# Kernel optimization log

Hardware: AMD Instinct MI355X
Metric: run time of the kernel (lower is better)

The kernel has to match this reference:

```python
import jax, jax.numpy as jnp
import numpy as np

H, D = 16, 64            # total_num_heads, head_dim
E = H * D                # embed_dim = 1024
NUM_BUCKETS, MAX_DIST = 32, 128
SCALING = D ** -0.5


def _rel_buckets(seq_len):
    # WavLM bidirectional relative position buckets (static, computed in numpy)
    ctx = np.arange(seq_len)[:, None]
    mem = np.arange(seq_len)[None, :]
    rel = mem - ctx                                  # [s, s]
    nb = NUM_BUCKETS // 2
    buckets = (rel > 0).astype(np.int64) * nb
    rp = np.abs(rel)
    max_exact = nb // 2
    is_small = rp < max_exact
    large = max_exact + (
        np.log(np.maximum(rp, 1) / max_exact) / np.log(MAX_DIST / max_exact) * (nb - max_exact)
    ).astype(np.int64)
    large = np.minimum(large, nb - 1)
    buckets = buckets + np.where(is_small, rp, large)
    return jnp.asarray(buckets)


def setup_inputs() -> dict:
    key = jax.random.key(0)
    ks = jax.random.split(key, 12)
    s = 0.02
    x = jax.random.normal(ks[0], (8, 1024, E), jnp.float32)
    Wq = jax.random.normal(ks[1], (E, H * D), jnp.float32) * s
    bq = jnp.zeros((H * D,), jnp.float32)
    Wk = jax.random.normal(ks[2], (E, H * D), jnp.float32) * s
    bk = jnp.zeros((H * D,), jnp.float32)
    Wv = jax.random.normal(ks[3], (E, H * D), jnp.float32) * s
    bv = jnp.zeros((H * D,), jnp.float32)
    Wo = jax.random.normal(ks[4], (H * D, E), jnp.float32) * s
    bo = jnp.zeros((E,), jnp.float32)
    rel_embed = jax.random.normal(ks[5], (NUM_BUCKETS, H), jnp.float32) * s
    gru_w = jax.random.normal(ks[6], (D, 8), jnp.float32) * s
    gru_b = jnp.zeros((8,), jnp.float32)
    gru_const = jnp.ones((1, H, 1, 1), jnp.float32)
    return {"x": x, "Wq": Wq, "bq": bq, "Wk": Wk, "bk": bk, "Wv": Wv, "bv": bv,
            "Wo": Wo, "bo": bo, "rel_embed": rel_embed,
            "gru_w": gru_w, "gru_b": gru_b, "gru_const": gru_const}


def reference(x, Wq, bq, Wk, bk, Wv, bv, Wo, bo, rel_embed, gru_w, gru_b, gru_const):
    b, s, e = x.shape
    # relative position bias: [H, s, s]
    buckets = _rel_buckets(s)
    pos_bias = jnp.transpose(rel_embed[buckets], (2, 0, 1))
    # gated relative position (gru_rel_pos)
    qlayer = x.reshape(b, s, H, D).transpose(0, 2, 1, 3)            # [b,H,s,D]
    g = jnp.einsum('bhsd,de->bhse', qlayer, gru_w) + gru_b          # [b,H,s,8]
    g = jax.nn.sigmoid(g.reshape(b, H, s, 2, 4).sum(-1))           # [b,H,s,2]
    gate_a, gate_b = g[..., :1], g[..., 1:]                         # [b,H,s,1]
    gate = gate_a * (gate_b * gru_const - 1.0) + 2.0                # [b,H,s,1]
    bias = gate * pos_bias[None]                                    # [b,H,s,s]
    # projections -> [b,H,s,D]
    q = (x @ Wq + bq).reshape(b, s, H, D).transpose(0, 2, 1, 3)
    k = (x @ Wk + bk).reshape(b, s, H, D).transpose(0, 2, 1, 3)
    v = (x @ Wv + bv).reshape(b, s, H, D).transpose(0, 2, 1, 3)
    scores = SCALING * jnp.einsum('bhqd,bhkd->bhqk', q, k) + bias
    w = jax.nn.softmax(scores, axis=-1)   # includes stable max-subtract
    out = jnp.einsum('bhqk,bhkd->bhqd', w, v)
    out = out.transpose(0, 2, 1, 3).reshape(b, s, H * D)
    return out @ Wo + bo
```

## Files before the change

### kernel.cpp

```cpp
#include <hip/hip_runtime.h>
#include <hip/hip_bf16.h>
#include <math.h>


typedef __attribute__((ext_vector_type(8))) short short8;
typedef __attribute__((ext_vector_type(4))) float f32x4;

#define LDSP(p) ((__attribute__((address_space(3))) void*)(p))
#define GLBP(p) ((const __attribute__((address_space(1))) void*)(p))

__device__ __forceinline__ void async_ld16(const void* src, void* dst) {
  __builtin_amdgcn_global_load_lds(GLBP(src), LDSP(dst), 16, 0, 0);
}
__device__ __forceinline__ unsigned short f2bf(float f) {
  __hip_bfloat16 h = __float2bfloat16(f);
  return __builtin_bit_cast(unsigned short, h);
}

__global__ void prep_btab(const float* __restrict__ rel_embed,
                          float* __restrict__ btab) {
  const int idx = blockIdx.x * 256 + threadIdx.x;
  if (idx >= 2047) return;
  const int rel = idx - 1023;
  int bucket = (rel > 0) ? 16 : 0;
  const int rp = rel < 0 ? -rel : rel;
  if (rp < 8) {
    bucket += rp;
  } else {
    const double lv = log((double)rp / 8.0) / log(16.0) * 8.0;
    int large = 8 + (int)lv;
    bucket += (large < 15) ? large : 15;
  }
  #pragma unroll
  for (int h = 0; h < 16; ++h)
    btab[h * 2048 + idx] = rel_embed[bucket * 16 + h];
}

__global__ __launch_bounds__(256) void cvt_gate(
    const float* __restrict__ x, const float* __restrict__ gw,
    const float* __restrict__ gb, const float* __restrict__ gcst,
    unsigned short* __restrict__ xb, float* __restrict__ gate_ws) {
  __shared__ __align__(16) float xr[1024];
  const int bs = blockIdx.x, t = threadIdx.x;
  const float4 v = *(const float4*)&x[(size_t)bs * 1024 + t * 4];
  *(float4*)&xr[t * 4] = v;
  ushort4 o;
  o.x = f2bf(v.x); o.y = f2bf(v.y); o.z = f2bf(v.z); o.w = f2bf(v.w);
  *(ushort4*)&xb[(size_t)bs * 1024 + t * 4] = o;
  __syncthreads();
  const int h = t >> 4, i = t & 15;
  float pa = 0.f, pb = 0.f;
  #pragma unroll
  for (int j = 0; j < 4; ++j) {
    const int d = i * 4 + j;
    const float xv = xr[h * 64 + d];
    const float* wr = &gw[d * 8];
    pa += xv * (wr[0] + wr[1] + wr[2] + wr[3]);
    pb += xv * (wr[4] + wr[5] + wr[6] + wr[7]);
  }
  #pragma unroll
  for (int msk = 1; msk <= 8; msk <<= 1) {
    pa += __shfl_xor(pa, msk);
    pb += __shfl_xor(pb, msk);
  }
  if (i == 0) {
    const float ba = gb[0] + gb[1] + gb[2] + gb[3];
    const float bb = gb[4] + gb[5] + gb[6] + gb[7];
    const float ga  = 1.f / (1.f + __expf(-(pa + ba)));
    const float gbv = 1.f / (1.f + __expf(-(pb + bb)));
    const float gv  = ga * (gbv * gcst[h] - 1.f) + 2.f;
    const int b = bs >> 10, s = bs & 1023;
    gate_ws[(b * 16 + h) * 1024 + s] = gv;
  }
}

__global__ __launch_bounds__(256) void transW4(
    const float* __restrict__ W0, const float* __restrict__ W1,
    const float* __restrict__ W2, const float* __restrict__ W3,
    unsigned short* __restrict__ Wt_all) {
  __shared__ __align__(16) float tile[64][68];
  const int z = blockIdx.z;
  const float* W = (z == 0) ? W0 : (z == 1) ? W1 : (z == 2) ? W2 : W3;
  unsigned short* Wt = Wt_all + (size_t)z * 1048576;
  const int n0 = blockIdx.x * 64, k0 = blockIdx.y * 64;
  const int c = (threadIdx.x & 15) * 4, r = threadIdx.x >> 4;
  #pragma unroll
  for (int i = 0; i < 4; ++i)
    *(float4*)&tile[r + i * 16][c] =
        *(const float4*)&W[(size_t)(k0 + r + i * 16) * 1024 + n0 + c];
  __syncthreads();
  #pragma unroll
  for (int i = 0; i < 4; ++i) {
    const int n = r + i * 16;
    ushort4 o;
    o.x = f2bf(tile[c + 0][n]); o.y = f2bf(tile[c + 1][n]);
    o.z = f2bf(tile[c + 2][n]); o.w = f2bf(tile[c + 3][n]);
    *(ushort4*)&Wt[(size_t)(n0 + n) * 1024 + k0 + c] = o;
  }
}

__device__ __forceinline__ void gemm_core(
    const unsigned short* __restrict__ A, const unsigned short* __restrict__ Bt,
    unsigned short* As, unsigned short* Bs, const int m0, const int n0,
    f32x4 acc[4][4]) {
  const int t = threadIdx.x, w = t >> 6, l = t & 63;
  const int lr = l & 15, lg = l >> 4;
  const int wr = w >> 1, wc = w & 1;

  const unsigned short* asrc[4];
  const unsigned short* bsrc[4];
  unsigned short* adst[4];
  unsigned short* bdst[4];
  #pragma unroll
  for (int i = 0; i < 4; ++i) {
    const int p = (w * 4 + i) * 64 + l, r = p >> 3, c = p & 7;
    const int cs = c ^ (r & 7);
    asrc[i] = A + (size_t)(m0 + r) * 1024 + cs * 8;
    bsrc[i] = Bt + (size_t)(n0 + r) * 1024 + cs * 8;
    adst[i] = &As[(w * 4 + i) * 512];
    bdst[i] = &Bs[(w * 4 + i) * 512];
  }

  int offA[2][4], offB[2][4];
  #pragma unroll
  for (int ks = 0; ks < 2; ++ks)
    #pragma unroll
    for (int mt = 0; mt < 4; ++mt) {
      offA[ks][mt] = (wr * 64 + mt * 16 + lr) * 64 + ((ks * 4 + lg) ^ (lr & 7)) * 8;
      offB[ks][mt] = (wc * 64 + mt * 16 + lr) * 64 + ((ks * 4 + lg) ^ (lr & 7)) * 8;
    }

  for (int k0 = 0; k0 < 16; ++k0) {
    #pragma unroll
    for (int i = 0; i < 4; ++i) {
      async_ld16(asrc[i], adst[i]);
      async_ld16(bsrc[i], bdst[i]);
      asrc[i] += 64;
      bsrc[i] += 64;
    }
    __syncthreads();
    #pragma unroll
    for (int ks = 0; ks < 2; ++ks) {
      short8 af[4], bf[4];
      #pragma unroll
      for (int mt = 0; mt < 4; ++mt) af[mt] = *(const short8*)&As[offA[ks][mt]];
      #pragma unroll
      for (int nt = 0; nt < 4; ++nt) bf[nt] = *(const short8*)&Bs[offB[ks][nt]];
      #pragma unroll
      for (int mt = 0; mt < 4; ++mt)
        #pragma unroll
        for (int nt = 0; nt < 4; ++nt)
          acc[mt][nt] = __builtin_amdgcn_mfma_f32_16x16x32_bf16(
              af[mt], bf[nt], acc[mt][nt], 0, 0, 0);
    }
    __syncthreads();
  }
}

__global__ __launch_bounds__(256) void gemm_qkv(
    const unsigned short* __restrict__ A, const unsigned short* __restrict__ wt_all,
    const float* __restrict__ bq, const float* __restrict__ bk,
    const float* __restrict__ bv, unsigned short* __restrict__ q_ws,
    unsigned short* __restrict__ k_ws, unsigned short* __restrict__ vt_ws) {
  __shared__ __align__(16) unsigned short As[128 * 64];
  __shared__ __align__(16) unsigned short Bs[128 * 64];
  const int which = blockIdx.y >> 3;
  const int m0 = blockIdx.x * 128, n0 = (blockIdx.y & 7) * 128;
  const unsigned short* Bt = wt_all + (size_t)which * 1048576;
  const float* bias = (which == 0) ? bq : (which == 1) ? bk : bv;

  f32x4 acc[4][4];
  #pragma unroll
  for (int mt = 0; mt < 4; ++mt)
    #pragma unroll
    for (int nt = 0; nt < 4; ++nt) acc[mt][nt] = (f32x4){0.f, 0.f, 0.f, 0.f};
  gemm_core(A, Bt, As, Bs, m0, n0, acc);

  const int t = threadIdx.x, w = t >> 6, l = t & 63;
  const int lr = l & 15, lg = l >> 4;
  const int wr = w >> 1, wc = w & 1;
  const int mbase = m0 + wr * 64, nbase = n0 + wc * 64;

  if (which == 2) {
    #pragma unroll
    for (int mt = 0; mt < 4; ++mt) {
      const int m4 = mbase + mt * 16 + lg * 4;
      const int b = m4 >> 10, s = m4 & 1023;
      #pragma unroll
      for (int nt = 0; nt < 4; ++nt) {
        const int n = nbase + nt * 16 + lr, h = n >> 6, d = n & 63;
        const float bvv = bias[n];
        ushort4 o;
        o.x = f2bf(acc[mt][nt][0] + bvv);
        o.y = f2bf(acc[mt][nt][1] + bvv);
        o.z = f2bf(acc[mt][nt][2] + bvv);
        o.w = f2bf(acc[mt][nt][3] + bvv);
        *(ushort4*)&vt_ws[(size_t)(b * 16 + h) * 65536 + (size_t)d * 1024 + s] = o;
      }
    }
  } else {
    unsigned short* dst = (which == 0) ? q_ws : k_ws;
    const float scale = (which == 0) ? 0.125f : 1.0f;
    #pragma unroll
    for (int mt = 0; mt < 4; ++mt)
      #pragma unroll
      for (int nt = 0; nt < 4; ++nt) {
        const int n = nbase + nt * 16 + lr, h = n >> 6, d = n & 63;
        const float bvv = bias[n];
        #pragma unroll
        for (int i = 0; i < 4; ++i) {
          const int m = mbase + mt * 16 + lg * 4 + i;
          const int b = m >> 10, s = m & 1023;
          dst[(size_t)(b * 16 + h) * 65536 + s * 64 + d] =
              f2bf((acc[mt][nt][i] + bvv) * scale);
        }
      }
  }
}

__global__ __launch_bounds__(256) void gemm_out(
    const unsigned short* __restrict__ A, const unsigned short* __restrict__ Bt,
    const float* __restrict__ bias, float* __restrict__ C) {
  __shared__ __align__(16) unsigned short As[128 * 64];
  __shared__ __align__(16) unsigned short Bs[128 * 64];
  const int m0 = blockIdx.x * 128, n0 = blockIdx.y * 128;
  f32x4 acc[4][4];
  #pragma unroll
  for (int mt = 0; mt < 4; ++mt)
    #pragma unroll
    for (int nt = 0; nt < 4; ++nt) acc[mt][nt] = (f32x4){0.f, 0.f, 0.f, 0.f};
  gemm_core(A, Bt, As, Bs, m0, n0, acc);

  const int t = threadIdx.x, w = t >> 6, l = t & 63;
  const int lr = l & 15, lg = l >> 4;
  const int wr = w >> 1, wc = w & 1;
  const int mbase = m0 + wr * 64, nbase = n0 + wc * 64;
  #pragma unroll
  for (int mt = 0; mt < 4; ++mt)
    #pragma unroll
    for (int nt = 0; nt < 4; ++nt) {
      const int n = nbase + nt * 16 + lr;
      const float bvv = bias[n];
      #pragma unroll
      for (int i = 0; i < 4; ++i) {
        const int m = mbase + mt * 16 + lg * 4 + i;
        C[(size_t)m * 1024 + n] = acc[mt][nt][i] + bvv;
      }
    }
}

__global__ __launch_bounds__(256) void attn_mfma(
    const unsigned short* __restrict__ q_ws, const unsigned short* __restrict__ k_ws,
    const unsigned short* __restrict__ vt_ws, const float* __restrict__ gate_ws,
    const float* __restrict__ btab, unsigned short* __restrict__ ctx) {
  __shared__ __align__(16) unsigned short Ks[2][64 * 64];
  __shared__ __align__(16) unsigned short Vts[2][64 * 64];
  __shared__ __align__(16) unsigned short QPs[64 * 64];
  __shared__ __align__(16) float biasl[1088];
  __shared__ float gates[64];
  __shared__ float scl[64];

  const int t = threadIdx.x, w = t >> 6, l = t & 63;
  const int lr = l & 15, lg = l >> 4;
  const int bh = blockIdx.x, h = bh & 15, b = bh >> 4;
  const int q0 = blockIdx.y * 64;
  const size_t hb = (size_t)bh * 65536;

  #pragma unroll
  for (int i = 0; i < 2; ++i) {
    const int p = (w * 2 + i) * 64 + l, r = p >> 3, c = p & 7;
    const int cs = c ^ (r & 7);
    async_ld16(q_ws + hb + (size_t)(q0 + r) * 64 + cs * 8, &QPs[(w * 2 + i) * 512]);
  }
  #pragma unroll
  for (int i = 0; i < 2; ++i) {
    const int p = (w * 2 + i) * 64 + l, r = p >> 3, c = p & 7;
    const int cs = c ^ (r & 7);
    async_ld16(k_ws + hb + (size_t)r * 64 + cs * 8, &Ks[0][(w * 2 + i) * 512]);
    async_ld16(vt_ws + hb + (size_t)r * 1024 + cs * 8, &Vts[0][(w * 2 + i) * 512]);
  }
  {
    const float* bt = btab + h * 2048 + (960 - q0);
    for (int u = t * 4; u < 1088; u += 1024)
      *(float4*)&biasl[u] = *(const float4*)&bt[u];
  }
  if (t < 64) gates[t] = gate_ws[bh * 1024 + q0 + t];
  __syncthreads();

  short8 qf[2];
  #pragma unroll
  for (int ks = 0; ks < 2; ++ks)
    qf[ks] = *(const short8*)&QPs[(w * 16 + lr) * 64 + ((ks * 4 + lg) ^ (lr & 7)) * 8];

  int pwoff[4], proff[2], offF[2][4];
  #pragma unroll
  for (int nt = 0; nt < 4; ++nt)
    pwoff[nt] = w * 2048 + ((lr * 128 + nt * 32 + lg * 8) ^ ((lr & 7) << 4));
  #pragma unroll
  for (int ks = 0; ks < 2; ++ks) {
    proff[ks] = w * 2048 + ((lr * 128 + ks * 64 + lg * 16) ^ ((lr & 7) << 4));
    #pragma unroll
    for (int nt = 0; nt < 4; ++nt)
      offF[ks][nt] = (nt * 16 + lr) * 64 + ((ks * 4 + lg) ^ (lr & 7)) * 8;
  }

  float mcur = -1e30f, lsum = 0.f;
  f32x4 acc_o[4];
  #pragma unroll
  for (int dt = 0; dt < 4; ++dt) acc_o[dt] = (f32x4){0.f, 0.f, 0.f, 0.f};
  const float gt = gates[w * 16 + lr];
  const int ub = 63 - w * 16 - lr;
  char* QPb = (char*)QPs;

  int cur = 0;
  for (int kt = 0; kt < 16; ++kt) {
    if (kt) {
      asm volatile("s_waitcnt vmcnt(0) lgkmcnt(0)" ::: "memory");
      __builtin_amdgcn_s_barrier();
      __builtin_amdgcn_sched_barrier(0);
    }
    if (kt + 1 < 16) {
      #pragma unroll
      for (int i = 0; i < 2; ++i) {
        const int p = (w * 2 + i) * 64 + l, r = p >> 3, c = p & 7;
        const int cs = c ^ (r & 7);
        async_ld16(k_ws + hb + (size_t)(kt + 1) * 4096 + (size_t)r * 64 + cs * 8,
                   &Ks[cur ^ 1][(w * 2 + i) * 512]);
        async_ld16(vt_ws + hb + (size_t)r * 1024 + (kt + 1) * 64 + cs * 8,
                   &Vts[cur ^ 1][(w * 2 + i) * 512]);
      }
    }

    f32x4 accs[4];
    #pragma unroll
    for (int nt = 0; nt < 4; ++nt) accs[nt] = (f32x4){0.f, 0.f, 0.f, 0.f};
    #pragma unroll
    for (int ks = 0; ks < 2; ++ks) {
      #pragma unroll
      for (int nt = 0; nt < 4; ++nt) {
        const short8 kf = *(const short8*)&Ks[cur][offF[ks][nt]];
        accs[nt] = __builtin_amdgcn_mfma_f32_16x16x32_bf16(kf, qf[ks], accs[nt], 0, 0, 0);
      }
    }

    const int bb = kt * 64 + ub + lg * 4;
    float tm = -1e30f;
    #pragma unroll
    for (int nt = 0; nt < 4; ++nt) {
      #pragma unroll
      for (int i = 0; i < 4; ++i) {
        const float sv = accs[nt][i] + gt * biasl[bb + nt * 16 + i];
        accs[nt][i] = sv;
        tm = fmaxf(tm, sv);
      }
    }
    tm = fmaxf(tm, __shfl_xor(tm, 16));
    tm = fmaxf(tm, __shfl_xor(tm, 32));

    const int skip = __all(tm <= mcur + 8.0f);
    float sc = 1.0f;
    if (!skip) {
      const float mn = fmaxf(mcur, tm);
      sc = __expf(mcur - mn);
      mcur = mn;
      if (lg == 0) scl[w * 16 + lr] = sc;
    }

    float ps = 0.f;
    #pragma unroll
    for (int nt = 0; nt < 4; ++nt) {
      float p0 = __expf(accs[nt][0] - mcur);
      float p1 = __expf(accs[nt][1] - mcur);
      float p2 = __expf(accs[nt][2] - mcur);
      float p3 = __expf(accs[nt][3] - mcur);
      ps += (p0 + p1) + (p2 + p3);
      short4 pk;
      pk.x = (short)f2bf(p0); pk.y = (short)f2bf(p1);
      pk.z = (short)f2bf(p2); pk.w = (short)f2bf(p3);
      *(short4*)(QPb + pwoff[nt]) = pk;
    }
    ps += __shfl_xor(ps, 16);
    ps += __shfl_xor(ps, 32);
    lsum = skip ? (lsum + ps) : (lsum * sc + ps);

    asm volatile("s_waitcnt lgkmcnt(0)" ::: "memory");
    __builtin_amdgcn_sched_barrier(0);

    if (!skip) {
      float s0 = scl[w * 16 + lg * 4 + 0];
      float s1 = scl[w * 16 + lg * 4 + 1];
      float s2 = scl[w * 16 + lg * 4 + 2];
      float s3 = scl[w * 16 + lg * 4 + 3];
      #pragma unroll
      for (int dt = 0; dt < 4; ++dt) {
        acc_o[dt][0] *= s0; acc_o[dt][1] *= s1;
        acc_o[dt][2] *= s2; acc_o[dt][3] *= s3;
      }
    }

    #pragma unroll
    for (int ks = 0; ks < 2; ++ks) {
      const short8 pf = *(const short8*)(QPb + proff[ks]);
      #pragma unroll
      for (int dt = 0; dt < 4; ++dt) {
        const short8 vf = *(const short8*)&Vts[cur][offF[ks][dt]];
        acc_o[dt] = __builtin_amdgcn_mfma_f32_16x16x32_bf16(pf, vf, acc_o[dt], 0, 0, 0);
      }
    }
    cur ^= 1;
  }

  if (lg == 0) scl[w * 16 + lr] = 1.0f / lsum;
  asm volatile("s_waitcnt lgkmcnt(0)" ::: "memory");
  __builtin_amdgcn_sched_barrier(0);
  float inv[4];
  #pragma unroll
  for (int i = 0; i < 4; ++i) inv[i] = scl[w * 16 + lg * 4 + i];
  #pragma unroll
  for (int i = 0; i < 4; ++i) {
    const int q = q0 + w * 16 + lg * 4 + i;
    const size_t rowoff = ((size_t)(b * 1024 + q) * 16 + h) * 64;
    #pragma unroll
    for (int dt = 0; dt < 4; ++dt)
      ctx[rowoff + dt * 16 + lr] = f2bf(acc_o[dt][i] * inv[i]);
  }
}

extern "C" void kernel_launch(void* const* d_in, const int* in_sizes, int n_in,
                              void* d_out, int out_size, void* d_ws, size_t ws_size,
                              hipStream_t stream) {
  const float* x    = (const float*)d_in[0];
  const float* Wq   = (const float*)d_in[1];
  const float* bq   = (const float*)d_in[2];
  const float* Wk   = (const float*)d_in[3];
  const float* bk   = (const float*)d_in[4];
  const float* Wv   = (const float*)d_in[5];
  const float* bv   = (const float*)d_in[6];
  const float* Wo   = (const float*)d_in[7];
  const float* bo   = (const float*)d_in[8];
  const float* rel  = (const float*)d_in[9];
  const float* gw   = (const float*)d_in[10];
  const float* gb   = (const float*)d_in[11];
  const float* gcst = (const float*)d_in[12];
  float* out = (float*)d_out;

  char* ws = (char*)d_ws;
  unsigned short* x_bf   = (unsigned short*)(ws);
  unsigned short* wt_all = (unsigned short*)(ws + 16777216);
  unsigned short* q_ws   = (unsigned short*)(ws + 25165824);
  unsigned short* k_ws   = (unsigned short*)(ws + 41943040);
  unsigned short* vt_ws  = (unsigned short*)(ws + 58720256);
  unsigned short* ctx    = (unsigned short*)(ws + 75497472);
  float* gate = (float*)(ws + 92274688);
  float* btab = (float*)(ws + 92798976);

  cvt_gate <<<dim3(8192),       256, 0, stream>>>(x, gw, gb, gcst, x_bf, gate);
  transW4  <<<dim3(16, 16, 4),  256, 0, stream>>>(Wq, Wk, Wv, Wo, wt_all);
  prep_btab<<<dim3(8),          256, 0, stream>>>(rel, btab);
  gemm_qkv <<<dim3(64, 24),     256, 0, stream>>>(x_bf, wt_all, bq, bk, bv,
                                                  q_ws, k_ws, vt_ws);
  attn_mfma<<<dim3(128, 16),    256, 0, stream>>>(q_ws, k_ws, vt_ws, gate, btab, ctx);
  gemm_out <<<dim3(64, 8),      256, 0, stream>>>(ctx, wt_all + 3 * 1048576, bo, out);
}
```

Before: 298.7 us.

## Merge prep kernels, use exp2 softmax, vectorize GEMM epilogues, restructure attention pipelining

Folds the three preprocessing kernels into one launch, which removes launch overhead. It swaps the MFMA operand order so the Q/K and output GEMM epilogues can write vectorized rows. The attention kernel folds log2(e) into the Q scale and gate so softmax can use exp2, and raises the rescale-skip threshold. It also loads Q straight into registers, single-buffers V with per-tile loads, and adds setprio around the MFMA blocks along with an extra barrier per iteration. The extra synchronization and loss of V double-buffering could cost overlap.

```diff
diff --git a/kernel.cpp b/kernel.cpp
--- a/kernel.cpp
+++ b/kernel.cpp
@@ -16,89 +16,95 @@
   __hip_bfloat16 h = __float2bfloat16(f);
   return __builtin_bit_cast(unsigned short, h);
 }
-
-__global__ void prep_btab(const float* __restrict__ rel_embed,
-                          float* __restrict__ btab) {
-  const int idx = blockIdx.x * 256 + threadIdx.x;
-  if (idx >= 2047) return;
-  const int rel = idx - 1023;
-  int bucket = (rel > 0) ? 16 : 0;
-  const int rp = rel < 0 ? -rel : rel;
-  if (rp < 8) {
-    bucket += rp;
-  } else {
-    const double lv = log((double)rp / 8.0) / log(16.0) * 8.0;
-    int large = 8 + (int)lv;
-    bucket += (large < 15) ? large : 15;
-  }
-  #pragma unroll
-  for (int h = 0; h < 16; ++h)
-    btab[h * 2048 + idx] = rel_embed[bucket * 16 + h];
-}
-
-__global__ __launch_bounds__(256) void cvt_gate(
+#if __has_builtin(__builtin_amdgcn_exp2f)
+#define EXP2(x) __builtin_amdgcn_exp2f(x)
+#else
+#define EXP2(x) exp2f(x)
+#endif
+
+__global__ __launch_bounds__(256) void prep_all(
     const float* __restrict__ x, const float* __restrict__ gw,
     const float* __restrict__ gb, const float* __restrict__ gcst,
-    unsigned short* __restrict__ xb, float* __restrict__ gate_ws) {
-  __shared__ __align__(16) float xr[1024];
-  const int bs = blockIdx.x, t = threadIdx.x;
-  const float4 v = *(const float4*)&x[(size_t)bs * 1024 + t * 4];
-  *(float4*)&xr[t * 4] = v;
-  ushort4 o;
-  o.x = f2bf(v.x); o.y = f2bf(v.y); o.z = f2bf(v.z); o.w = f2bf(v.w);
-  *(ushort4*)&xb[(size_t)bs * 1024 + t * 4] = o;
-  __syncthreads();
-  const int h = t >> 4, i = t & 15;
-  float pa = 0.f, pb = 0.f;
-  #pragma unroll
-  for (int j = 0; j < 4; ++j) {
-    const int d = i * 4 + j;
-    const float xv = xr[h * 64 + d];
-    const float* wr = &gw[d * 8];
-    pa += xv * (wr[0] + wr[1] + wr[2] + wr[3]);
-    pb += xv * (wr[4] + wr[5] + wr[6] + wr[7]);
-  }
-  #pragma unroll
-  for (int msk = 1; msk <= 8; msk <<= 1) {
-    pa += __shfl_xor(pa, msk);
-    pb += __shfl_xor(pb, msk);
-  }
-  if (i == 0) {
-    const float ba = gb[0] + gb[1] + gb[2] + gb[3];
-    const float bb = gb[4] + gb[5] + gb[6] + gb[7];
-    const float ga  = 1.f / (1.f + __expf(-(pa + ba)));
-    const float gbv = 1.f / (1.f + __expf(-(pb + bb)));
-    const float gv  = ga * (gbv * gcst[h] - 1.f) + 2.f;
-    const int b = bs >> 10, s = bs & 1023;
-    gate_ws[(b * 16 + h) * 1024 + s] = gv;
-  }
-}
-
-__global__ __launch_bounds__(256) void transW4(
     const float* __restrict__ W0, const float* __restrict__ W1,
     const float* __restrict__ W2, const float* __restrict__ W3,
-    unsigned short* __restrict__ Wt_all) {
+    const float* __restrict__ rel_embed,
+    unsigned short* __restrict__ xb, float* __restrict__ gate_ws,
+    unsigned short* __restrict__ Wt_all, float* __restrict__ btab) {
   __shared__ __align__(16) float tile[64][68];
-  const int z = blockIdx.z;
-  const float* W = (z == 0) ? W0 : (z == 1) ? W1 : (z == 2) ? W2 : W3;
-  unsigned short* Wt = Wt_all + (size_t)z * 1048576;
-  const int n0 = blockIdx.x * 64, k0 = blockIdx.y * 64;
-  const int c = (threadIdx.x & 15) * 4, r = threadIdx.x >> 4;
-  #pragma unroll
-  for (int i = 0; i < 4; ++i)
-    *(float4*)&tile[r + i * 16][c] =
-        *(const float4*)&W[(size_t)(k0 + r + i * 16) * 1024 + n0 + c];
-  __syncthreads();
-  #pragma unroll
-  for (int i = 0; i < 4; ++i) {
-    const int n = r + i * 16;
+  const int bid = blockIdx.x, t = threadIdx.x;
+  if (bid < 8192) {
+    float* xr = &tile[0][0];
+    const float4 v = *(const float4*)&x[(size_t)bid * 1024 + t * 4];
+    *(float4*)&xr[t * 4] = v;
     ushort4 o;
-    o.x = f2bf(tile[c + 0][n]); o.y = f2bf(tile[c + 1][n]);
-    o.z = f2bf(tile[c + 2][n]); o.w = f2bf(tile[c + 3][n]);
-    *(ushort4*)&Wt[(size_t)(n0 + n) * 1024 + k0 + c] = o;
-  }
-}
-
+    o.x = f2bf(v.x); o.y = f2bf(v.y); o.z = f2bf(v.z); o.w = f2bf(v.w);
+    *(ushort4*)&xb[(size_t)bid * 1024 + t * 4] = o;
+    __syncthreads();
+    const int h = t >> 4, i = t & 15;
+    float pa = 0.f, pb = 0.f;
+    #pragma unroll
+    for (int j = 0; j < 4; ++j) {
+      const int d = i * 4 + j;
+      const float xv = xr[h * 64 + d];
+      const float* wr = &gw[d * 8];
+      pa += xv * (wr[0] + wr[1] + wr[2] + wr[3]);
+      pb += xv * (wr[4] + wr[5] + wr[6] + wr[7]);
+    }
+    #pragma unroll
+    for (int msk = 1; msk <= 8; msk <<= 1) {
+      pa += __shfl_xor(pa, msk);
+      pb += __shfl_xor(pb, msk);
+    }
+    if (i == 0) {
+      const float ba = gb[0] + gb[1] + gb[2] + gb[3];
+      const float bb = gb[4] + gb[5] + gb[6] + gb[7];
+      const float ga  = 1.f / (1.f + __expf(-(pa + ba)));
+      const float gbv = 1.f / (1.f + __expf(-(pb + bb)));
+      const float gv  = ga * (gbv * gcst[h] - 1.f) + 2.f;
+      const int b = bid >> 10, s = bid & 1023;
+      gate_ws[(b * 16 + h) * 1024 + s] = gv;
+    }
+  } else if (bid < 9216) {
+    const int zz = bid - 8192;
+    const int z = zz >> 8;
+    const float* W = (z == 0) ? W0 : (z == 1) ? W1 : (z == 2) ? W2 : W3;
+    unsigned short* Wt = Wt_all + (size_t)z * 1048576;
+    const int n0 = (zz & 15) * 64, k0 = ((zz >> 4) & 15) * 64;
+    const int c = (t & 15) * 4, r = t >> 4;
+    #pragma unroll
+    for (int i = 0; i < 4; ++i)
+      *(float4*)&tile[r + i * 16][c] =
+          *(const float4*)&W[(size_t)(k0 + r + i * 16) * 1024 + n0 + c];
+    __syncthreads();
+    #pragma unroll
+    for (int i = 0; i < 4; ++i) {
+      const int n = r + i * 16;
+      ushort4 o;
+      o.x = f2bf(tile[c + 0][n]); o.y = f2bf(tile[c + 1][n]);
+      o.z = f2bf(tile[c + 2][n]); o.w = f2bf(tile[c + 3][n]);
+      *(ushort4*)&Wt[(size_t)(n0 + n) * 1024 + k0 + c] = o;
+    }
+  } else {
+    const int idx = (bid - 9216) * 256 + t;
+    if (idx < 2047) {
+      const int rel = idx - 1023;
+      int bucket = (rel > 0) ? 16 : 0;
+      const int rp = rel < 0 ? -rel : rel;
+      if (rp < 8) {
+        bucket += rp;
+      } else {
+        const double lv = log((double)rp / 8.0) / log(16.0) * 8.0;
+        int large = 8 + (int)lv;
+        bucket += (large < 15) ? large : 15;
+      }
+      #pragma unroll
+      for (int h = 0; h < 16; ++h)
+        btab[h * 2048 + idx] = rel_embed[bucket * 16 + h];
+    }
+  }
+}
+
+template <int SWAP>
 __device__ __forceinline__ void gemm_core(
     const unsigned short* __restrict__ A, const unsigned short* __restrict__ Bt,
     unsigned short* As, unsigned short* Bs, const int m0, const int n0,
@@ -150,8 +156,9 @@
       for (int mt = 0; mt < 4; ++mt)
         #pragma unroll
         for (int nt = 0; nt < 4; ++nt)
-          acc[mt][nt] = __builtin_amdgcn_mfma_f32_16x16x32_bf16(
-              af[mt], bf[nt], acc[mt][nt], 0, 0, 0);
+          acc[mt][nt] = SWAP
+              ? __builtin_amdgcn_mfma_f32_16x16x32_bf16(bf[nt], af[mt], acc[mt][nt], 0, 0, 0)
+              : __builtin_amdgcn_mfma_f32_16x16x32_bf16(af[mt], bf[nt], acc[mt][nt], 0, 0, 0);
     }
     __syncthreads();
   }
@@ -167,21 +174,20 @@
   const int which = blockIdx.y >> 3;
   const int m0 = blockIdx.x * 128, n0 = (blockIdx.y & 7) * 128;
   const unsigned short* Bt = wt_all + (size_t)which * 1048576;
-  const float* bias = (which == 0) ? bq : (which == 1) ? bk : bv;
-
-  f32x4 acc[4][4];
-  #pragma unroll
-  for (int mt = 0; mt < 4; ++mt)
-    #pragma unroll
-    for (int nt = 0; nt < 4; ++nt) acc[mt][nt] = (f32x4){0.f, 0.f, 0.f, 0.f};
-  gemm_core(A, Bt, As, Bs, m0, n0, acc);
 
   const int t = threadIdx.x, w = t >> 6, l = t & 63;
   const int lr = l & 15, lg = l >> 4;
   const int wr = w >> 1, wc = w & 1;
   const int mbase = m0 + wr * 64, nbase = n0 + wc * 64;
 
+  f32x4 acc[4][4];
+  #pragma unroll
+  for (int mt = 0; mt < 4; ++mt)
+    #pragma unroll
+    for (int nt = 0; nt < 4; ++nt) acc[mt][nt] = (f32x4){0.f, 0.f, 0.f, 0.f};
+
   if (which == 2) {
+    gemm_core<0>(A, Bt, As, Bs, m0, n0, acc);
     #pragma unroll
     for (int mt = 0; mt < 4; ++mt) {
       const int m4 = mbase + mt * 16 + lg * 4;
@@ -189,7 +195,7 @@
       #pragma unroll
       for (int nt = 0; nt < 4; ++nt) {
         const int n = nbase + nt * 16 + lr, h = n >> 6, d = n & 63;
-        const float bvv = bias[n];
+        const float bvv = bv[n];
         ushort4 o;
         o.x = f2bf(acc[mt][nt][0] + bvv);
         o.y = f2bf(acc[mt][nt][1] + bvv);
@@ -199,22 +205,27 @@
       }
     }
   } else {
+    gemm_core<1>(A, Bt, As, Bs, m0, n0, acc);
     unsigned short* dst = (which == 0) ? q_ws : k_ws;
-    const float scale = (which == 0) ? 0.125f : 1.0f;
-    #pragma unroll
-    for (int mt = 0; mt < 4; ++mt)
-      #pragma unroll
-      for (int nt = 0; nt < 4; ++nt) {
-        const int n = nbase + nt * 16 + lr, h = n >> 6, d = n & 63;
-        const float bvv = bias[n];
-        #pragma unroll
-        for (int i = 0; i < 4; ++i) {
-          const int m = mbase + mt * 16 + lg * 4 + i;
-          const int b = m >> 10, s = m & 1023;
-          dst[(size_t)(b * 16 + h) * 65536 + s * 64 + d] =
-              f2bf((acc[mt][nt][i] + bvv) * scale);
-        }
-      }
+    const float* bias = (which == 0) ? bq : bk;
+    const float scale = (which == 0) ? 0.18033688011f : 1.0f;
+    #pragma unroll
+    for (int nt = 0; nt < 4; ++nt) {
+      const int n4 = nbase + nt * 16 + lg * 4;
+      const int h = n4 >> 6, d = n4 & 63;
+      const float4 b4 = *(const float4*)&bias[n4];
+      #pragma unroll
+      for (int mt = 0; mt < 4; ++mt) {
+        const int m = mbase + mt * 16 + lr;
+        const int b = m >> 10, s = m & 1023;
+        ushort4 o;
+        o.x = f2bf((acc[mt][nt][0] + b4.x) * scale);
+        o.y = f2bf((acc[mt][nt][1] + b4.y) * scale);
+        o.z = f2bf((acc[mt][nt][2] + b4.z) * scale);
+        o.w = f2bf((acc[mt][nt][3] + b4.w) * scale);
+        *(ushort4*)&dst[(size_t)(b * 16 + h) * 65536 + s * 64 + d] = o;
+      }
+    }
   }
 }
 
@@ -229,24 +240,27 @@
   for (int mt = 0; mt < 4; ++mt)
     #pragma unroll
     for (int nt = 0; nt < 4; ++nt) acc[mt][nt] = (f32x4){0.f, 0.f, 0.f, 0.f};
-  gemm_core(A, Bt, As, Bs, m0, n0, acc);
+  gemm_core<1>(A, Bt, As, Bs, m0, n0, acc);
 
   const int t = threadIdx.x, w = t >> 6, l = t & 63;
   const int lr = l & 15, lg = l >> 4;
   const int wr = w >> 1, wc = w & 1;
   const int mbase = m0 + wr * 64, nbase = n0 + wc * 64;
   #pragma unroll
-  for (int mt = 0; mt < 4; ++mt)
-    #pragma unroll
-    for (int nt = 0; nt < 4; ++nt) {
-      const int n = nbase + nt * 16 + lr;
-      const float bvv = bias[n];
-      #pragma unroll
-      for (int i = 0; i < 4; ++i) {
-        const int m = mbase + mt * 16 + lg * 4 + i;
-        C[(size_t)m * 1024 + n] = acc[mt][nt][i] + bvv;
-      }
-    }
+  for (int nt = 0; nt < 4; ++nt) {
+    const int n4 = nbase + nt * 16 + lg * 4;
+    const float4 b4 = *(const float4*)&bias[n4];
+    #pragma unroll
+    for (int mt = 0; mt < 4; ++mt) {
+      const int m = mbase + mt * 16 + lr;
+      float4 o;
+      o.x = acc[mt][nt][0] + b4.x;
+      o.y = acc[mt][nt][1] + b4.y;
+      o.z = acc[mt][nt][2] + b4.z;
+      o.w = acc[mt][nt][3] + b4.w;
+      *(float4*)&C[(size_t)m * 1024 + n4] = o;
+    }
+  }
 }
 
 __global__ __launch_bounds__(256) void attn_mfma(
@@ -254,8 +268,8 @@
     const unsigned short* __restrict__ vt_ws, const float* __restrict__ gate_ws,
     const float* __restrict__ btab, unsigned short* __restrict__ ctx) {
   __shared__ __align__(16) unsigned short Ks[2][64 * 64];
-  __shared__ __align__(16) unsigned short Vts[2][64 * 64];
-  __shared__ __align__(16) unsigned short QPs[64 * 64];
+  __shared__ __align__(16) unsigned short Vts[64 * 64];
+  __shared__ __align__(16) unsigned short Ps[4 * 1024];
   __shared__ __align__(16) float biasl[1088];
   __shared__ float gates[64];
   __shared__ float scl[64];
@@ -266,18 +280,17 @@
   const int q0 = blockIdx.y * 64;
   const size_t hb = (size_t)bh * 65536;
 
-  #pragma unroll
-  for (int i = 0; i < 2; ++i) {
-    const int p = (w * 2 + i) * 64 + l, r = p >> 3, c = p & 7;
-    const int cs = c ^ (r & 7);
-    async_ld16(q_ws + hb + (size_t)(q0 + r) * 64 + cs * 8, &QPs[(w * 2 + i) * 512]);
-  }
+  short8 qf[2];
+  #pragma unroll
+  for (int ks = 0; ks < 2; ++ks)
+    qf[ks] = *(const short8*)(q_ws + hb + (size_t)(q0 + w * 16 + lr) * 64 +
+                              (ks * 4 + lg) * 8);
+
   #pragma unroll
   for (int i = 0; i < 2; ++i) {
     const int p = (w * 2 + i) * 64 + l, r = p >> 3, c = p & 7;
     const int cs = c ^ (r & 7);
     async_ld16(k_ws + hb + (size_t)r * 64 + cs * 8, &Ks[0][(w * 2 + i) * 512]);
-    async_ld16(vt_ws + hb + (size_t)r * 1024 + cs * 8, &Vts[0][(w * 2 + i) * 512]);
   }
   {
     const float* bt = btab + h * 2048 + (960 - q0);
@@ -285,12 +298,9 @@
       *(float4*)&biasl[u] = *(const float4*)&bt[u];
   }
   if (t < 64) gates[t] = gate_ws[bh * 1024 + q0 + t];
-  __syncthreads();
-
-  short8 qf[2];
-  #pragma unroll
-  for (int ks = 0; ks < 2; ++ks)
-    qf[ks] = *(const short8*)&QPs[(w * 16 + lr) * 64 + ((ks * 4 + lg) ^ (lr & 7)) * 8];
+  asm volatile("s_waitcnt vmcnt(0) lgkmcnt(0)" ::: "memory");
+  __builtin_amdgcn_s_barrier();
+  __builtin_amdgcn_sched_barrier(0);
 
   int pwoff[4], proff[2], offF[2][4];
   #pragma unroll
@@ -308,40 +318,42 @@
   f32x4 acc_o[4];
   #pragma unroll
   for (int dt = 0; dt < 4; ++dt) acc_o[dt] = (f32x4){0.f, 0.f, 0.f, 0.f};
-  const float gt = gates[w * 16 + lr];
+  const float gtl = gates[w * 16 + lr] * 1.44269504f;
   const int ub = 63 - w * 16 - lr;
-  char* QPb = (char*)QPs;
-
-  int cur = 0;
+  char* Pb = (char*)Ps;
+
+  int pcur = 0;
   for (int kt = 0; kt < 16; ++kt) {
-    if (kt) {
-      asm volatile("s_waitcnt vmcnt(0) lgkmcnt(0)" ::: "memory");
-      __builtin_amdgcn_s_barrier();
-      __builtin_amdgcn_sched_barrier(0);
-    }
-    if (kt + 1 < 16) {
+    #pragma unroll
+    for (int i = 0; i < 2; ++i) {
+      const int p = (w * 2 + i) * 64 + l, r = p >> 3, c = p & 7;
+      const int cs = c ^ (r & 7);
+      async_ld16(vt_ws + hb + (size_t)r * 1024 + kt * 64 + cs * 8,
+                 &Vts[(w * 2 + i) * 512]);
+    }
+    if (kt < 15) {
       #pragma unroll
       for (int i = 0; i < 2; ++i) {
         const int p = (w * 2 + i) * 64 + l, r = p >> 3, c = p & 7;
         const int cs = c ^ (r & 7);
         async_ld16(k_ws + hb + (size_t)(kt + 1) * 4096 + (size_t)r * 64 + cs * 8,
-                   &Ks[cur ^ 1][(w * 2 + i) * 512]);
-        async_ld16(vt_ws + hb + (size_t)r * 1024 + (kt + 1) * 64 + cs * 8,
-                   &Vts[cur ^ 1][(w * 2 + i) * 512]);
+                   &Ks[pcur ^ 1][(w * 2 + i) * 512]);
       }
     }
 
     f32x4 accs[4];
     #pragma unroll
     for (int nt = 0; nt < 4; ++nt) accs[nt] = (f32x4){0.f, 0.f, 0.f, 0.f};
+    __builtin_amdgcn_s_setprio(1);
     #pragma unroll
     for (int ks = 0; ks < 2; ++ks) {
       #pragma unroll
       for (int nt = 0; nt < 4; ++nt) {
-        const short8 kf = *(const short8*)&Ks[cur][offF[ks][nt]];
+        const short8 kf = *(const short8*)&Ks[pcur][offF[ks][nt]];
         accs[nt] = __builtin_amdgcn_mfma_f32_16x16x32_bf16(kf, qf[ks], accs[nt], 0, 0, 0);
       }
     }
+    __builtin_amdgcn_s_setprio(0);
 
     const int bb = kt * 64 + ub + lg * 4;
     float tm = -1e30f;
@@ -349,19 +361,20 @@
     for (int nt = 0; nt < 4; ++nt) {
       #pragma unroll
       for (int i = 0; i < 4; ++i) {
-        const float sv = accs[nt][i] + gt * biasl[bb + nt * 16 + i];
+        const float sv = accs[nt][i] + gtl * biasl[bb + nt * 16 + i];
         accs[nt][i] = sv;
-        tm = fmaxf(tm, sv);
-      }
+      }
+      tm = fmaxf(fmaxf(tm, fmaxf(accs[nt][0], accs[nt][1])),
+                 fmaxf(accs[nt][2], accs[nt][3]));
     }
     tm = fmaxf(tm, __shfl_xor(tm, 16));
     tm = fmaxf(tm, __shfl_xor(tm, 32));
 
-    const int skip = __all(tm <= mcur + 8.0f);
+    const int skip = __all(tm <= mcur + 11.5f);
     float sc = 1.0f;
     if (!skip) {
       const float mn = fmaxf(mcur, tm);
-      sc = __expf(mcur - mn);
+      sc = EXP2(mcur - mn);
       mcur = mn;
       if (lg == 0) scl[w * 16 + lr] = sc;
     }
@@ -369,28 +382,33 @@
     float ps = 0.f;
     #pragma unroll
     for (int nt = 0; nt < 4; ++nt) {
-      float p0 = __expf(accs[nt][0] - mcur);
-      float p1 = __expf(accs[nt][1] - mcur);
-      float p2 = __expf(accs[nt][2] - mcur);
-      float p3 = __expf(accs[nt][3] - mcur);
+      const float p0 = EXP2(accs[nt][0] - mcur);
+      const float p1 = EXP2(accs[nt][1] - mcur);
+      const float p2 = EXP2(accs[nt][2] - mcur);
+      const float p3 = EXP2(accs[nt][3] - mcur);
       ps += (p0 + p1) + (p2 + p3);
       short4 pk;
       pk.x = (short)f2bf(p0); pk.y = (short)f2bf(p1);
       pk.z = (short)f2bf(p2); pk.w = (short)f2bf(p3);
-      *(short4*)(QPb + pwoff[nt]) = pk;
+      *(short4*)(Pb + pwoff[nt]) = pk;
     }
     ps += __shfl_xor(ps, 16);
     ps += __shfl_xor(ps, 32);
     lsum = skip ? (lsum + ps) : (lsum * sc + ps);
 
-    asm volatile("s_waitcnt lgkmcnt(0)" ::: "memory");
+    if (kt < 15) {
+      asm volatile("s_waitcnt vmcnt(2) lgkmcnt(0)" ::: "memory");
+    } else {
+      asm volatile("s_waitcnt vmcnt(0) lgkmcnt(0)" ::: "memory");
+    }
+    __builtin_amdgcn_s_barrier();
     __builtin_amdgcn_sched_barrier(0);
 
     if (!skip) {
-      float s0 = scl[w * 16 + lg * 4 + 0];
-      float s1 = scl[w * 16 + lg * 4 + 1];
-      float s2 = scl[w * 16 + lg * 4 + 2];
-      float s3 = scl[w * 16 + lg * 4 + 3];
+      const float s0 = scl[w * 16 + lg * 4 + 0];
+      const float s1 = scl[w * 16 + lg * 4 + 1];
+      const float s2 = scl[w * 16 + lg * 4 + 2];
+      const float s3 = scl[w * 16 + lg * 4 + 3];
       #pragma unroll
       for (int dt = 0; dt < 4; ++dt) {
         acc_o[dt][0] *= s0; acc_o[dt][1] *= s1;
@@ -398,16 +416,22 @@
       }
     }
 
+    __builtin_amdgcn_s_setprio(1);
     #pragma unroll
     for (int ks = 0; ks < 2; ++ks) {
-      const short8 pf = *(const short8*)(QPb + proff[ks]);
+      const short8 pf = *(const short8*)(Pb + proff[ks]);
       #pragma unroll
       for (int dt = 0; dt < 4; ++dt) {
-        const short8 vf = *(const short8*)&Vts[cur][offF[ks][dt]];
+        const short8 vf = *(const short8*)&Vts[offF[ks][dt]];
         acc_o[dt] = __builtin_amdgcn_mfma_f32_16x16x32_bf16(pf, vf, acc_o[dt], 0, 0, 0);
       }
     }
-    cur ^= 1;
+    __builtin_amdgcn_s_setprio(0);
+
+    asm volatile("s_waitcnt vmcnt(0)" ::: "memory");
+    __builtin_amdgcn_s_barrier();
+    __builtin_amdgcn_sched_barrier(0);
+    pcur ^= 1;
   }
 
   if (lg == 0) scl[w * 16 + lr] = 1.0f / lsum;
@@ -454,11 +478,10 @@
   float* gate = (float*)(ws + 92274688);
   float* btab = (float*)(ws + 92798976);
 
-  cvt_gate <<<dim3(8192),       256, 0, stream>>>(x, gw, gb, gcst, x_bf, gate);
-  transW4  <<<dim3(16, 16, 4),  256, 0, stream>>>(Wq, Wk, Wv, Wo, wt_all);
-  prep_btab<<<dim3(8),          256, 0, stream>>>(rel, btab);
-  gemm_qkv <<<dim3(64, 24),     256, 0, stream>>>(x_bf, wt_all, bq, bk, bv,
-                                                  q_ws, k_ws, vt_ws);
-  attn_mfma<<<dim3(128, 16),    256, 0, stream>>>(q_ws, k_ws, vt_ws, gate, btab, ctx);
-  gemm_out <<<dim3(64, 8),      256, 0, stream>>>(ctx, wt_all + 3 * 1048576, bo, out);
-}
+  prep_all <<<dim3(9224),    256, 0, stream>>>(x, gw, gb, gcst, Wq, Wk, Wv, Wo,
+                                               rel, x_bf, gate, wt_all, btab);
+  gemm_qkv <<<dim3(64, 24),  256, 0, stream>>>(x_bf, wt_all, bq, bk, bv,
+                                               q_ws, k_ws, vt_ws);
+  attn_mfma<<<dim3(128, 16), 256, 0, stream>>>(q_ws, k_ws, vt_ws, gate, btab, ctx);
+  gemm_out <<<dim3(64, 8),   256, 0, stream>>>(ctx, wt_all + 3 * 1048576, bo, out);
+}
```

Result: faster. 292.0 us (-2.2%).
